# Kernel tuning notes

Measured on AMD Instinct MI355X. Metric: run time of the kernel, lower is better.

The kernel has to match this reference:

```python
import jax, jax.numpy as jnp
import numpy as np

EPS = 1e-5

def conv1x1(x, w):
    # x: (B,C,H,W), w: (O,C) -> (B,O,H,W)
    return jnp.einsum('bchw,oc->bohw', x, w)

def bn_relu(y, g, b, m, v):
    s = g / jnp.sqrt(v + EPS)
    return jax.nn.relu(y * s[None, :, None, None] + (b - m * s)[None, :, None, None])

def cbr(x, w, g, b, m, v):
    return bn_relu(conv1x1(x, w), g, b, m, v)

def _bn_params(key, c):
    k1, k2, k3, k4 = jax.random.split(key, 4)
    g = 1.0 + 0.1 * jax.random.normal(k1, (c,), jnp.float32)
    b = 0.1 * jax.random.normal(k2, (c,), jnp.float32)
    m = 0.05 * jax.random.normal(k3, (c,), jnp.float32)
    v = jax.random.uniform(k4, (c,), jnp.float32, 0.5, 1.5)
    return g, b, m, v

def setup_inputs() -> dict:
    key = jax.random.key(0)
    B, Cin, H, W = 8, 512, 64, 64
    Ck, Cv, Cout = 256, 256, 512
    ks = jax.random.split(key, 12)
    def w(k, o, c):
        return jax.random.normal(k, (o, c), jnp.float32) * (1.0 / np.sqrt(c))
    inp = {}
    inp['x'] = jax.random.normal(ks[0], (B, Cin, H, W), jnp.float32)
    # f_key
    inp['kW1'] = w(ks[1], Ck, Cin); inp['kG1'], inp['kB1'], inp['kM1'], inp['kV1'] = _bn_params(ks[2], Ck)
    inp['kW2'] = w(ks[3], Ck, Ck);  inp['kG2'], inp['kB2'], inp['kM2'], inp['kV2'] = _bn_params(ks[4], Ck)
    # f_query
    inp['qW1'] = w(ks[5], Ck, Cin); inp['qG1'], inp['qB1'], inp['qM1'], inp['qV1'] = _bn_params(ks[6], Ck)
    inp['qW2'] = w(ks[7], Ck, Ck);  inp['qG2'], inp['qB2'], inp['qM2'], inp['qV2'] = _bn_params(ks[8], Ck)
    # f_value
    inp['vW'] = w(ks[9], Cv, Cin)
    # W (output projection)
    inp['wW'] = w(ks[10], Cout, Cv); inp['wG'], inp['wB'], inp['wM'], inp['wV'] = _bn_params(ks[11], Cout)
    return inp

def reference(x,
              kW1, kG1, kB1, kM1, kV1, kW2, kG2, kB2, kM2, kV2,
              qW1, qG1, qB1, qM1, qV1, qW2, qG2, qB2, qM2, qV2,
              vW,
              wW, wG, wB, wM, wV):
    B, _, H, W = x.shape
    q = cbr(cbr(x, qW1, qG1, qB1, qM1, qV1), qW2, qG2, qB2, qM2, qV2)  # (B,Ck,H,W)
    k = cbr(cbr(x, kW1, kG1, kB1, kM1, kV1), kW2, kG2, kB2, kM2, kV2)  # (B,Ck,H,W)
    v = conv1x1(x, vW)                                                  # (B,Cv,H,W)
    Ck = q.shape[1]; Cv = v.shape[1]; N = H * W
    qf = q.reshape(B, Ck, N)   # query = qf^T -> (B,N,Ck)
    kf = k.reshape(B, Ck, N)
    vf = v.reshape(B, Cv, N)
    sim = jnp.einsum('bcn,bcm->bnm', qf, kf) * (Ck ** -0.5)  # (B,N,N)
    attn = jax.nn.softmax(sim, axis=-1)
    ctx = jnp.einsum('bnm,bcm->bcn', attn, vf).reshape(B, Cv, H, W)
    return cbr(ctx, wW, wG, wB, wM, wV)
```

## Files before the change

kernel.cpp:

```cpp
#include <hip/hip_runtime.h>
#include <hip/hip_bf16.h>

typedef __attribute__((ext_vector_type(8))) short bf16x8;
typedef __attribute__((ext_vector_type(4))) float f32x4;

#define MFMA16(a, b, c) __builtin_amdgcn_mfma_f32_16x16x32_bf16(a, b, c, 0, 0, 0)

static __device__ __forceinline__ unsigned short f2bf(float f) {
  union { __hip_bfloat16 h; unsigned short u; } cv;
  cv.h = __float2bfloat16(f);
  return cv.u;
}

static __device__ __forceinline__ void gload16(const void* gptr, void* lptr) {
  __builtin_amdgcn_global_load_lds(
      (const __attribute__((address_space(1))) void*)gptr,
      (__attribute__((address_space(3))) void*)lptr, 16, 0, 0);
}


__global__ void conv_w_k(const float* __restrict__ qW1, const float* __restrict__ kW1,
                         const float* __restrict__ qW2, const float* __restrict__ kW2,
                         const float* __restrict__ vW, const float* __restrict__ wW,
                         __hip_bfloat16* __restrict__ dst) {
  int i = blockIdx.x * 256 + threadIdx.x;
  const float* src; int off;
  if (i < 131072)      { src = qW1; off = i; }
  else if (i < 262144) { src = kW1; off = i - 131072; }
  else if (i < 327680) { src = qW2; off = i - 262144; }
  else if (i < 393216) { src = kW2; off = i - 327680; }
  else if (i < 524288) { src = vW;  off = i - 393216; }
  else                 { src = wW;  off = i - 524288; }
  dst[i] = __float2bfloat16(src[off]);
}

__global__ void bn_all_k(const float* __restrict__ qG1, const float* __restrict__ qB1, const float* __restrict__ qM1, const float* __restrict__ qV1,
                         const float* __restrict__ qG2, const float* __restrict__ qB2, const float* __restrict__ qM2, const float* __restrict__ qV2,
                         const float* __restrict__ kG1, const float* __restrict__ kB1, const float* __restrict__ kM1, const float* __restrict__ kV1,
                         const float* __restrict__ kG2, const float* __restrict__ kB2, const float* __restrict__ kM2, const float* __restrict__ kV2,
                         const float* __restrict__ wG, const float* __restrict__ wB, const float* __restrict__ wM, const float* __restrict__ wV,
                         float* __restrict__ base) {
  int bidx = blockIdx.x, tid = threadIdx.x;
  const float *g, *b, *m, *v; float *s, *t; int i;
  if (bidx == 0)      { g = qG1; b = qB1; m = qM1; v = qV1; s = base;        t = base + 256;  i = tid; }
  else if (bidx == 1) { g = qG2; b = qB2; m = qM2; v = qV2; s = base + 512;  t = base + 768;  i = tid; }
  else if (bidx == 2) { g = kG1; b = kB1; m = kM1; v = kV1; s = base + 1024; t = base + 1280; i = tid; }
  else if (bidx == 3) { g = kG2; b = kB2; m = kM2; v = kV2; s = base + 1536; t = base + 1792; i = tid; }
  else                { g = wG;  b = wB;  m = wM;  v = wV;  s = base + 2048; t = base + 2560; i = (bidx - 4) * 256 + tid; }
  float sv = g[i] * rsqrtf(v[i] + 1e-5f);
  s[i] = sv;
  t[i] = b[i] - m[i] * sv;
}

__global__ __launch_bounds__(256) void transpose_k(const float* __restrict__ x,
                                                   __hip_bfloat16* __restrict__ xT) {
  __shared__ float tile[64][65];
  const int n0 = blockIdx.x * 64, c0 = blockIdx.y * 64, b = blockIdx.z;
  const int tx = threadIdx.x, ty = threadIdx.y;
  const float* xp = x + ((size_t)(b * 512 + c0) * 4096) + n0;
#pragma unroll
  for (int i = 0; i < 16; ++i) {
    int c = ty + 4 * i;
    tile[c][tx] = xp[(size_t)c * 4096 + tx];
  }
  __syncthreads();
  __hip_bfloat16* op = xT + ((size_t)(b * 4096 + n0) * 512) + c0;
#pragma unroll
  for (int i = 0; i < 16; ++i) {
    int nl = ty + 4 * i;
    op[(size_t)nl * 512 + tx] = __float2bfloat16(tile[tx][nl]);
  }
}

template <int EPI>
__global__ __launch_bounds__(256) void gemm_nt_k(
    const __hip_bfloat16* __restrict__ A, long sA,
    const __hip_bfloat16* __restrict__ B, long sB,
    void* __restrict__ Cp, long sC,
    int lda, int ldb, int ldc, int K,
    const float* __restrict__ s, const float* __restrict__ t) {
  __shared__ short As[128][72];
  __shared__ short Bs[128][72];
  const int tid = threadIdx.x;
  const int w = tid >> 6, l = tid & 63, g = l >> 4, ln = l & 15;
  const int wr = w >> 1, wc = w & 1;
  const int rb = blockIdx.x * 128, cb = blockIdx.y * 128;
  const __hip_bfloat16* Ab = A + (size_t)blockIdx.z * sA;
  const __hip_bfloat16* Bb = B + (size_t)blockIdx.z * sB;

  f32x4 acc[4][4];
#pragma unroll
  for (int i = 0; i < 4; ++i)
#pragma unroll
    for (int j = 0; j < 4; ++j) acc[i][j] = (f32x4){0.f, 0.f, 0.f, 0.f};

  const int r0 = tid >> 3;
  const int c8 = (tid & 7) * 8;

  for (int k0 = 0; k0 < K; k0 += 64) {
#pragma unroll
    for (int i = 0; i < 4; ++i) {
      const int r = r0 + 32 * i;
      *(uint4*)&As[r][c8] = *(const uint4*)(Ab + (size_t)(rb + r) * lda + (k0 + c8));
      *(uint4*)&Bs[r][c8] = *(const uint4*)(Bb + (size_t)(cb + r) * ldb + (k0 + c8));
    }
    __syncthreads();
#pragma unroll
    for (int kk = 0; kk < 2; ++kk) {
      bf16x8 av[4], bv[4];
#pragma unroll
      for (int i = 0; i < 4; ++i) av[i] = *(const bf16x8*)&As[64 * wr + 16 * i + ln][32 * kk + 8 * g];
#pragma unroll
      for (int i = 0; i < 4; ++i) bv[i] = *(const bf16x8*)&Bs[64 * wc + 16 * i + ln][32 * kk + 8 * g];
#pragma unroll
      for (int mi = 0; mi < 4; ++mi)
#pragma unroll
        for (int ni = 0; ni < 4; ++ni)
          acc[mi][ni] = MFMA16(av[mi], bv[ni], acc[mi][ni]);
    }
    __syncthreads();
  }

  const int row0 = rb + 64 * wr + 4 * g;
  const int col0 = cb + 64 * wc + ln;

  if (EPI == 2) {
    float* C = (float*)Cp + (size_t)blockIdx.z * sC;
#pragma unroll
    for (int mi = 0; mi < 4; ++mi) {
#pragma unroll
      for (int r = 0; r < 4; ++r) {
        const int R = row0 + 16 * mi + r;
        const float sr = s[R], tr = t[R];
#pragma unroll
        for (int ni = 0; ni < 4; ++ni) {
          float v = fmaf(acc[mi][ni][r], sr, tr);
          C[(size_t)R * ldc + (col0 + 16 * ni)] = v > 0.f ? v : 0.f;
        }
      }
    }
  } else {
    __hip_bfloat16* C = (__hip_bfloat16*)Cp + (size_t)blockIdx.z * sC;
    float sc[4], tc[4];
    if (EPI == 1) {
#pragma unroll
      for (int ni = 0; ni < 4; ++ni) { sc[ni] = s[col0 + 16 * ni]; tc[ni] = t[col0 + 16 * ni]; }
    }
#pragma unroll
    for (int mi = 0; mi < 4; ++mi) {
#pragma unroll
      for (int ni = 0; ni < 4; ++ni) {
#pragma unroll
        for (int r = 0; r < 4; ++r) {
          float v = acc[mi][ni][r];
          if (EPI == 1) { v = fmaf(v, sc[ni], tc[ni]); v = v > 0.f ? v : 0.f; }
          C[(size_t)(row0 + 16 * mi + r) * ldc + (col0 + 16 * ni)] = __float2bfloat16(v);
        }
      }
    }
  }
}

__global__ __launch_bounds__(256, 2) void flash_k(
    const __hip_bfloat16* __restrict__ Q,
    const __hip_bfloat16* __restrict__ Kt,
    const __hip_bfloat16* __restrict__ V,
    __hip_bfloat16* __restrict__ O) {
  __shared__ short Ks[64 * 256];
  __shared__ short Vs[256 * 64];
  __shared__ char Ps[4][2048];

  const int tid = threadIdx.x;
  const int w = tid >> 6, l = tid & 63, g = l >> 4, ln = l & 15;
  const int bid = blockIdx.x;
  const int batch = bid & 7;
  const int qb = (bid >> 3) << 6;
  const size_t bo = (size_t)batch * (4096 * 256);
  const float CE = 0.09016844005556021f;

  const int swz45 = (16 * g) ^ ((ln & 3) << 4);
  const int s6 = ((ln >> 2) & 1) << 6;
  const char* Ks0 = (const char*)Ks + (ln * 512 + swz45 + s6);
  const char* Ks1 = Ks0 + ((((ln >> 2) & 1) ? -64 : 64));
  const char* Vs0 = (const char*)Vs + (ln * 128 + swz45 + s6);
  const char* Vs1 = Vs0 + ((((ln >> 2) & 1) ? -64 : 64));
  const char* Pr0 = Ps[w] + (ln * 128 + swz45 + s6);
  const char* Pr1 = Pr0 + ((((ln >> 2) & 1) ? -64 : 64));
  const int pwOff = ln * 128 + 8 * (g & 1) + (((g >> 1) ^ (ln & 1)) << 4) +
                    (((ln >> 1) & 1) << 5) + s6;

  bf16x8 qf[8];
  {
    const __hip_bfloat16* qp = Q + bo + (size_t)(qb + 16 * w + ln) * 256 + 8 * g;
#pragma unroll
    for (int kk = 0; kk < 8; ++kk) qf[kk] = *(const bf16x8*)(qp + 32 * kk);
  }

  f32x4 acc[16];
#pragma unroll
  for (int ci = 0; ci < 16; ++ci) acc[ci] = (f32x4){0.f, 0.f, 0.f, 0.f};
  float m_run = -1e30f, l_run = 0.f;

  const int kRow = 16 * w + (l >> 5);
  const int kChunk = (l & 31) ^ (l >> 5);
  const int vRow = 64 * w + (l >> 3);
  const int vChunk = (l & 7) ^ ((l >> 3) & 7);

  const short* Kb = (const short*)(Kt + bo);
  const short* Vb = (const short*)(V + bo);

  auto stageK = [&](int m0) {
#pragma unroll
    for (int j = 0; j < 8; ++j) {
      const short* gp = Kb + (size_t)(m0 + kRow + 2 * j) * 256 + 8 * (kChunk ^ ((2 * j) & 7));
      gload16(gp, Ks + w * 4096 + j * 512);
    }
  };
  auto stageV = [&](int m0) {
#pragma unroll
    for (int j = 0; j < 8; ++j) {
      const short* gp = Vb + (size_t)(vRow + 8 * j) * 4096 + m0 + 8 * vChunk;
      gload16(gp, Vs + w * 4096 + j * 512);
    }
  };

  stageK(0);
  stageV(0);
  __builtin_amdgcn_sched_barrier(0);

  for (int t = 0; t < 64; ++t) {
    asm volatile("s_waitcnt vmcnt(8)" ::: "memory");
    __builtin_amdgcn_sched_barrier(0);
    __builtin_amdgcn_s_barrier();
    __builtin_amdgcn_sched_barrier(0);

    f32x4 sf[4];
#pragma unroll
    for (int mi = 0; mi < 4; ++mi) sf[mi] = (f32x4){0.f, 0.f, 0.f, 0.f};
    __builtin_amdgcn_s_setprio(1);
#pragma unroll
    for (int kk = 0; kk < 8; ++kk) {
      const char* kp = ((kk & 1) ? Ks1 : Ks0) + 128 * (kk >> 1);
#pragma unroll
      for (int mi = 0; mi < 4; ++mi) {
        bf16x8 a = *(const bf16x8*)(kp + 8192 * mi);
        sf[mi] = MFMA16(a, qf[kk], sf[mi]);
      }
    }
    __builtin_amdgcn_s_setprio(0);

    float sv[16];
#pragma unroll
    for (int mi = 0; mi < 4; ++mi)
#pragma unroll
      for (int r = 0; r < 4; ++r) sv[4 * mi + r] = sf[mi][r];
    float a0 = fmaxf(fmaxf(sv[0], sv[1]), sv[2]);
    float a1 = fmaxf(fmaxf(sv[3], sv[4]), sv[5]);
    float a2 = fmaxf(fmaxf(sv[6], sv[7]), sv[8]);
    float a3 = fmaxf(fmaxf(sv[9], sv[10]), sv[11]);
    float a4 = fmaxf(fmaxf(sv[12], sv[13]), sv[14]);
    float mmax = fmaxf(fmaxf(fmaxf(fmaxf(a0, a1), a2), fmaxf(a3, a4)), sv[15]);
    mmax = fmaxf(mmax, __shfl_xor(mmax, 16));
    mmax = fmaxf(mmax, __shfl_xor(mmax, 32));

    if (!__all((mmax - m_run) * CE <= 8.0f)) {
      float m_new = fmaxf(m_run, mmax);
      float alpha = exp2f((m_run - m_new) * CE);
      l_run *= alpha;
#pragma unroll
      for (int r = 0; r < 4; ++r) {
        float ar = __shfl(alpha, 4 * g + r);
#pragma unroll
        for (int ci = 0; ci < 16; ++ci) acc[ci][r] *= ar;
      }
      m_run = m_new;
    }
    float p[16], psum = 0.f;
#pragma unroll
    for (int j = 0; j < 16; ++j) {
      p[j] = exp2f((sv[j] - m_run) * CE);
      psum += p[j];
    }
    psum += __shfl_xor(psum, 16);
    psum += __shfl_xor(psum, 32);
    l_run += psum;

    {
      uint2 pk0, pk1, pk2, pk3;
      pk0.x = (unsigned int)f2bf(p[0])  | ((unsigned int)f2bf(p[1])  << 16);
      pk0.y = (unsigned int)f2bf(p[2])  | ((unsigned int)f2bf(p[3])  << 16);
      pk1.x = (unsigned int)f2bf(p[4])  | ((unsigned int)f2bf(p[5])  << 16);
      pk1.y = (unsigned int)f2bf(p[6])  | ((unsigned int)f2bf(p[7])  << 16);
      pk2.x = (unsigned int)f2bf(p[8])  | ((unsigned int)f2bf(p[9])  << 16);
      pk2.y = (unsigned int)f2bf(p[10]) | ((unsigned int)f2bf(p[11]) << 16);
      pk3.x = (unsigned int)f2bf(p[12]) | ((unsigned int)f2bf(p[13]) << 16);
      pk3.y = (unsigned int)f2bf(p[14]) | ((unsigned int)f2bf(p[15]) << 16);
      *(uint2*)(Ps[w] + (pwOff ^ 0))  = pk0;
      *(uint2*)(Ps[w] + (pwOff ^ 32)) = pk1;
      *(uint2*)(Ps[w] + (pwOff ^ 64)) = pk2;
      *(uint2*)(Ps[w] + (pwOff ^ 96)) = pk3;
    }

    asm volatile("s_waitcnt vmcnt(0)" ::: "memory");
    __builtin_amdgcn_sched_barrier(0);
    __builtin_amdgcn_s_barrier();
    __builtin_amdgcn_sched_barrier(0);

    if (t < 63) stageK(64 * (t + 1));
    __builtin_amdgcn_sched_barrier(0);

    __builtin_amdgcn_s_setprio(1);
#pragma unroll
    for (int kk2 = 0; kk2 < 2; ++kk2) {
      bf16x8 pa = *(const bf16x8*)(kk2 ? Pr1 : Pr0);
#pragma unroll
      for (int ci = 0; ci < 16; ++ci) {
        bf16x8 vfr = *(const bf16x8*)((kk2 ? Vs1 : Vs0) + 2048 * ci);
        acc[ci] = MFMA16(pa, vfr, acc[ci]);
      }
    }
    __builtin_amdgcn_s_setprio(0);

    __builtin_amdgcn_s_barrier();
    __builtin_amdgcn_sched_barrier(0);
    if (t < 63) stageV(64 * (t + 1));
    __builtin_amdgcn_sched_barrier(0);
  }

  float linv[4];
#pragma unroll
  for (int r = 0; r < 4; ++r) linv[r] = 1.0f / __shfl(l_run, 4 * g + r);

  __hip_bfloat16* Ob = O + bo;
#pragma unroll
  for (int ci = 0; ci < 16; ++ci) {
#pragma unroll
    for (int r = 0; r < 4; ++r) {
      float val = acc[ci][r] * linv[r];
      Ob[(size_t)(qb + 16 * w + 4 * g + r) * 256 + 16 * ci + ln] = __float2bfloat16(val);
    }
  }
}


extern "C" void kernel_launch(void* const* d_in, const int* in_sizes, int n_in,
                              void* d_out, int out_size, void* d_ws, size_t ws_size,
                              hipStream_t stream) {
  const float* x   = (const float*)d_in[0];
  const float* kW1 = (const float*)d_in[1];
  const float* kG1 = (const float*)d_in[2];
  const float* kB1 = (const float*)d_in[3];
  const float* kM1 = (const float*)d_in[4];
  const float* kV1 = (const float*)d_in[5];
  const float* kW2 = (const float*)d_in[6];
  const float* kG2 = (const float*)d_in[7];
  const float* kB2 = (const float*)d_in[8];
  const float* kM2 = (const float*)d_in[9];
  const float* kV2 = (const float*)d_in[10];
  const float* qW1 = (const float*)d_in[11];
  const float* qG1 = (const float*)d_in[12];
  const float* qB1 = (const float*)d_in[13];
  const float* qM1 = (const float*)d_in[14];
  const float* qV1 = (const float*)d_in[15];
  const float* qW2 = (const float*)d_in[16];
  const float* qG2 = (const float*)d_in[17];
  const float* qB2 = (const float*)d_in[18];
  const float* qM2 = (const float*)d_in[19];
  const float* qV2 = (const float*)d_in[20];
  const float* vW  = (const float*)d_in[21];
  const float* wW  = (const float*)d_in[22];
  const float* wG  = (const float*)d_in[23];
  const float* wB  = (const float*)d_in[24];
  const float* wM  = (const float*)d_in[25];
  const float* wV  = (const float*)d_in[26];

  char* ws = (char*)d_ws;
  __hip_bfloat16* bQW1 = (__hip_bfloat16*)(ws + 0);
  __hip_bfloat16* bKW1 = (__hip_bfloat16*)(ws + 262144);
  __hip_bfloat16* bQW2 = (__hip_bfloat16*)(ws + 524288);
  __hip_bfloat16* bKW2 = (__hip_bfloat16*)(ws + 655360);
  __hip_bfloat16* bVW  = (__hip_bfloat16*)(ws + 786432);
  __hip_bfloat16* bWW  = (__hip_bfloat16*)(ws + 1048576);
  float* bnBase = (float*)(ws + 1310720);
  float* sQ1 = bnBase + 0;
  float* tQ1 = bnBase + 256;
  float* sQ2 = bnBase + 512;
  float* tQ2 = bnBase + 768;
  float* sK1 = bnBase + 1024;
  float* tK1 = bnBase + 1280;
  float* sK2 = bnBase + 1536;
  float* tK2 = bnBase + 1792;
  float* sWo = bnBase + 2048;
  float* tWo = bnBase + 2560;
  __hip_bfloat16* xT   = (__hip_bfloat16*)(ws + 2097152);
  __hip_bfloat16* bufA = (__hip_bfloat16*)(ws + 35651584);
  __hip_bfloat16* q2b  = (__hip_bfloat16*)(ws + 52428800);
  __hip_bfloat16* k2b  = (__hip_bfloat16*)(ws + 69206016);
  __hip_bfloat16* vB   = (__hip_bfloat16*)(ws + 85983232);

  conv_w_k<<<2560, 256, 0, stream>>>(qW1, kW1, qW2, kW2, vW, wW, bQW1);
  bn_all_k<<<6, 256, 0, stream>>>(qG1, qB1, qM1, qV1, qG2, qB2, qM2, qV2,
                                  kG1, kB1, kM1, kV1, kG2, kB2, kM2, kV2,
                                  wG, wB, wM, wV, bnBase);

  transpose_k<<<dim3(64, 8, 8), dim3(64, 4), 0, stream>>>(x, xT);

  gemm_nt_k<1><<<dim3(32, 2, 8), 256, 0, stream>>>(xT, 2097152L, bQW1, 0L, bufA, 1048576L,
                                                   512, 512, 256, 512, sQ1, tQ1);
  gemm_nt_k<1><<<dim3(32, 2, 8), 256, 0, stream>>>(bufA, 1048576L, bQW2, 0L, q2b, 1048576L,
                                                   256, 256, 256, 256, sQ2, tQ2);
  gemm_nt_k<1><<<dim3(32, 2, 8), 256, 0, stream>>>(xT, 2097152L, bKW1, 0L, bufA, 1048576L,
                                                   512, 512, 256, 512, sK1, tK1);
  gemm_nt_k<1><<<dim3(32, 2, 8), 256, 0, stream>>>(bufA, 1048576L, bKW2, 0L, k2b, 1048576L,
                                                   256, 256, 256, 256, sK2, tK2);
  gemm_nt_k<0><<<dim3(2, 32, 8), 256, 0, stream>>>(bVW, 0L, xT, 2097152L, vB, 1048576L,
                                                   512, 512, 4096, 512, nullptr, nullptr);
  flash_k<<<512, 256, 0, stream>>>(q2b, k2b, vB, bufA);
  gemm_nt_k<2><<<dim3(4, 32, 8), 256, 0, stream>>>(bWW, 0L, bufA, 1048576L, d_out, 2097152L,
                                                   256, 256, 4096, 256, sWo, tWo);
}
```

Measured before the change: 296.7 us.

## Split PV output channels across waves and load V fragments directly to registers

```diff
diff --git a/kernel.cpp b/kernel.cpp
--- a/kernel.cpp
+++ b/kernel.cpp
@@ -167,8 +167,10 @@
     const __hip_bfloat16* __restrict__ V,
     __hip_bfloat16* __restrict__ O) {
   __shared__ short Ks[64 * 256];
-  __shared__ short Vs[256 * 64];
-  __shared__ char Ps[4][2048];
+  __shared__ short Ps[64 * 64];
+  __shared__ float aLds[64];
+  __shared__ float lLds[64];
+  __shared__ int fLds[4];
 
   const int tid = threadIdx.x;
   const int w = tid >> 6, l = tid & 63, g = l >> 4, ln = l & 15;
@@ -181,12 +183,10 @@
   const int swz45 = (16 * g) ^ ((ln & 3) << 4);
   const int s6 = ((ln >> 2) & 1) << 6;
   const char* Ks0 = (const char*)Ks + (ln * 512 + swz45 + s6);
-  const char* Ks1 = Ks0 + ((((ln >> 2) & 1) ? -64 : 64));
-  const char* Vs0 = (const char*)Vs + (ln * 128 + swz45 + s6);
-  const char* Vs1 = Vs0 + ((((ln >> 2) & 1) ? -64 : 64));
-  const char* Pr0 = Ps[w] + (ln * 128 + swz45 + s6);
-  const char* Pr1 = Pr0 + ((((ln >> 2) & 1) ? -64 : 64));
-  const int pwOff = ln * 128 + 8 * (g & 1) + (((g >> 1) ^ (ln & 1)) << 4) +
+  const char* Ks1 = Ks0 + (((ln >> 2) & 1) ? -64 : 64);
+  const char* Pr0 = (const char*)Ps + (ln * 128 + swz45 + s6);
+  const char* Pr1 = Pr0 + (((ln >> 2) & 1) ? -64 : 64);
+  const int pwOff = (16 * w + ln) * 128 + 8 * (g & 1) + (((g >> 1) ^ (ln & 1)) << 4) +
                     (((ln >> 1) & 1) << 5) + s6;
 
   bf16x8 qf[8];
@@ -196,18 +196,17 @@
     for (int kk = 0; kk < 8; ++kk) qf[kk] = *(const bf16x8*)(qp + 32 * kk);
   }
 
-  f32x4 acc[16];
-#pragma unroll
-  for (int ci = 0; ci < 16; ++ci) acc[ci] = (f32x4){0.f, 0.f, 0.f, 0.f};
+  f32x4 acc[4][4];
+#pragma unroll
+  for (int qg = 0; qg < 4; ++qg)
+#pragma unroll
+    for (int ci = 0; ci < 4; ++ci) acc[qg][ci] = (f32x4){0.f, 0.f, 0.f, 0.f};
   float m_run = -1e30f, l_run = 0.f;
 
   const int kRow = 16 * w + (l >> 5);
   const int kChunk = (l & 31) ^ (l >> 5);
-  const int vRow = 64 * w + (l >> 3);
-  const int vChunk = (l & 7) ^ ((l >> 3) & 7);
-
   const short* Kb = (const short*)(Kt + bo);
-  const short* Vb = (const short*)(V + bo);
+  const short* Vp = (const short*)(V + bo) + (size_t)(64 * w + ln) * 4096 + 8 * g;
 
   auto stageK = [&](int m0) {
 #pragma unroll
@@ -216,22 +215,27 @@
       gload16(gp, Ks + w * 4096 + j * 512);
     }
   };
-  auto stageV = [&](int m0) {
-#pragma unroll
-    for (int j = 0; j < 8; ++j) {
-      const short* gp = Vb + (size_t)(vRow + 8 * j) * 4096 + m0 + 8 * vChunk;
-      gload16(gp, Vs + w * 4096 + j * 512);
-    }
-  };
 
   stageK(0);
-  stageV(0);
   __builtin_amdgcn_sched_barrier(0);
 
   for (int t = 0; t < 64; ++t) {
+    const int m0 = t << 6;
+
+    bf16x8 vfr[8];
+#pragma unroll
+    for (int ci = 0; ci < 4; ++ci)
+#pragma unroll
+      for (int kk = 0; kk < 2; ++kk) {
+        const short* gp = Vp + (size_t)ci * (16 * 4096) + (m0 + 32 * kk);
+        asm volatile("global_load_dwordx4 %0, %1, off" : "=v"(vfr[2 * ci + kk]) : "v"(gp));
+      }
+    __builtin_amdgcn_sched_barrier(0);
+
     asm volatile("s_waitcnt vmcnt(8)" ::: "memory");
     __builtin_amdgcn_sched_barrier(0);
     __builtin_amdgcn_s_barrier();
+    asm volatile("" ::: "memory");
     __builtin_amdgcn_sched_barrier(0);
 
     f32x4 sf[4];
@@ -263,17 +267,14 @@
     mmax = fmaxf(mmax, __shfl_xor(mmax, 16));
     mmax = fmaxf(mmax, __shfl_xor(mmax, 32));
 
+    float alpha = 1.0f;
+    int rs = 0;
     if (!__all((mmax - m_run) * CE <= 8.0f)) {
       float m_new = fmaxf(m_run, mmax);
-      float alpha = exp2f((m_run - m_new) * CE);
+      alpha = exp2f((m_run - m_new) * CE);
       l_run *= alpha;
-#pragma unroll
-      for (int r = 0; r < 4; ++r) {
-        float ar = __shfl(alpha, 4 * g + r);
-#pragma unroll
-        for (int ci = 0; ci < 16; ++ci) acc[ci][r] *= ar;
-      }
       m_run = m_new;
+      rs = 1;
     }
     float p[16], psum = 0.f;
 #pragma unroll
@@ -295,49 +296,77 @@
       pk2.y = (unsigned int)f2bf(p[10]) | ((unsigned int)f2bf(p[11]) << 16);
       pk3.x = (unsigned int)f2bf(p[12]) | ((unsigned int)f2bf(p[13]) << 16);
       pk3.y = (unsigned int)f2bf(p[14]) | ((unsigned int)f2bf(p[15]) << 16);
-      *(uint2*)(Ps[w] + (pwOff ^ 0))  = pk0;
-      *(uint2*)(Ps[w] + (pwOff ^ 32)) = pk1;
-      *(uint2*)(Ps[w] + (pwOff ^ 64)) = pk2;
-      *(uint2*)(Ps[w] + (pwOff ^ 96)) = pk3;
-    }
-
-    asm volatile("s_waitcnt vmcnt(0)" ::: "memory");
+      char* Pb = (char*)Ps;
+      *(uint2*)(Pb + (pwOff ^ 0))  = pk0;
+      *(uint2*)(Pb + (pwOff ^ 32)) = pk1;
+      *(uint2*)(Pb + (pwOff ^ 64)) = pk2;
+      *(uint2*)(Pb + (pwOff ^ 96)) = pk3;
+    }
+    if (g == 0) aLds[16 * w + ln] = alpha;
+    if (l == 0) fLds[w] = rs;
+
+    asm volatile("" ::: "memory");
     __builtin_amdgcn_sched_barrier(0);
     __builtin_amdgcn_s_barrier();
-    __builtin_amdgcn_sched_barrier(0);
-
-    if (t < 63) stageK(64 * (t + 1));
+    asm volatile("" ::: "memory");
+    __builtin_amdgcn_sched_barrier(0);
+
+    if (t < 63) stageK(m0 + 64);
+    __builtin_amdgcn_sched_barrier(0);
+
+    {
+      int4 fl = *(const int4*)fLds;
+      if (fl.x | fl.y | fl.z | fl.w) {
+#pragma unroll
+        for (int qg = 0; qg < 4; ++qg) {
+          f32x4 av = *(const f32x4*)&aLds[16 * qg + 4 * g];
+#pragma unroll
+          for (int ci = 0; ci < 4; ++ci) acc[qg][ci] *= av;
+        }
+      }
+    }
+
+    if (t < 63) {
+      asm volatile("s_waitcnt vmcnt(8)" ::: "memory");
+    } else {
+      asm volatile("s_waitcnt vmcnt(0)" ::: "memory");
+    }
     __builtin_amdgcn_sched_barrier(0);
 
     __builtin_amdgcn_s_setprio(1);
 #pragma unroll
-    for (int kk2 = 0; kk2 < 2; ++kk2) {
-      bf16x8 pa = *(const bf16x8*)(kk2 ? Pr1 : Pr0);
-#pragma unroll
-      for (int ci = 0; ci < 16; ++ci) {
-        bf16x8 vfr = *(const bf16x8*)((kk2 ? Vs1 : Vs0) + 2048 * ci);
-        acc[ci] = MFMA16(pa, vfr, acc[ci]);
+    for (int kk = 0; kk < 2; ++kk) {
+#pragma unroll
+      for (int qg = 0; qg < 4; ++qg) {
+        bf16x8 pa = *(const bf16x8*)((kk ? Pr1 : Pr0) + 2048 * qg);
+#pragma unroll
+        for (int ci = 0; ci < 4; ++ci)
+          acc[qg][ci] = MFMA16(pa, vfr[2 * ci + kk], acc[qg][ci]);
       }
     }
     __builtin_amdgcn_s_setprio(0);
-
-    __builtin_amdgcn_s_barrier();
-    __builtin_amdgcn_sched_barrier(0);
-    if (t < 63) stageV(64 * (t + 1));
-    __builtin_amdgcn_sched_barrier(0);
-  }
-
-  float linv[4];
-#pragma unroll
-  for (int r = 0; r < 4; ++r) linv[r] = 1.0f / __shfl(l_run, 4 * g + r);
+    __builtin_amdgcn_sched_barrier(0);
+  }
+
+  if (g == 0) lLds[16 * w + ln] = l_run;
+  asm volatile("" ::: "memory");
+  __builtin_amdgcn_s_barrier();
+  asm volatile("" ::: "memory");
 
   __hip_bfloat16* Ob = O + bo;
 #pragma unroll
-  for (int ci = 0; ci < 16; ++ci) {
-#pragma unroll
-    for (int r = 0; r < 4; ++r) {
-      float val = acc[ci][r] * linv[r];
-      Ob[(size_t)(qb + 16 * w + 4 * g + r) * 256 + 16 * ci + ln] = __float2bfloat16(val);
+  for (int qg = 0; qg < 4; ++qg) {
+    f32x4 lv = *(const f32x4*)&lLds[16 * qg + 4 * g];
+    f32x4 li;
+#pragma unroll
+    for (int r = 0; r < 4; ++r) li[r] = 1.0f / lv[r];
+#pragma unroll
+    for (int ci = 0; ci < 4; ++ci) {
+#pragma unroll
+      for (int r = 0; r < 4; ++r) {
+        float val = acc[qg][ci][r] * li[r];
+        Ob[(size_t)(qb + 16 * qg + 4 * g + r) * 256 + 64 * w + 16 * ci + ln] = __float2bfloat16(val);
+      }
     }
   }
 }
```

Result: slower. 308.4 us (+3.9%).
